# Performance work log

Hardware: AMD Instinct MI355X
Metric: run time of the kernel (lower is better)

Reference implementation:

```python
import jax, jax.numpy as jnp
import numpy as np

BERT_VOCAB_SIZE = 28996
INPUT_SIZE = 768
HIDDEN = 512
BI_H = 2 * HIDDEN


def _gru_cell(x, h, wih, whh, bih, bhh):
    # PyTorch GRUCell math. x: [I], h: [H]; wih: [3H, I], whh: [3H, H]
    H = h.shape[-1]
    gx = wih @ x + bih            # [3H]
    gh = whh @ h + bhh            # [3H]
    r = jax.nn.sigmoid(gx[:H] + gh[:H])
    z = jax.nn.sigmoid(gx[H:2 * H] + gh[H:2 * H])
    n = jnp.tanh(gx[2 * H:] + r * gh[2 * H:])
    return (1.0 - z) * n + z * h


def _run_gru(xs, h0, wih, whh, bih, bhh):
    def step(h, x):
        hn = _gru_cell(x, h, wih, whh, bih, bhh)
        return hn, hn
    _, hs = jax.lax.scan(step, h0, xs)
    return hs  # [L, H]


def setup_inputs() -> dict:
    key = jax.random.key(0)
    ks = jax.random.split(key, 16)
    s = 0.02
    inp = {
        'input_context': jax.random.normal(ks[0], (512, INPUT_SIZE), jnp.float32),
        'output_context': jax.random.normal(ks[1], (1024, INPUT_SIZE), jnp.float32),
        # forward encoder GRUCell
        'fw_wih': jax.random.normal(ks[2], (3 * HIDDEN, INPUT_SIZE), jnp.float32) * s,
        'fw_whh': jax.random.normal(ks[3], (3 * HIDDEN, HIDDEN), jnp.float32) * s,
        'fw_bih': jnp.zeros((3 * HIDDEN,), jnp.float32),
        'fw_bhh': jnp.zeros((3 * HIDDEN,), jnp.float32),
        # backward encoder GRUCell
        'bw_wih': jax.random.normal(ks[4], (3 * HIDDEN, INPUT_SIZE), jnp.float32) * s,
        'bw_whh': jax.random.normal(ks[5], (3 * HIDDEN, HIDDEN), jnp.float32) * s,
        'bw_bih': jnp.zeros((3 * HIDDEN,), jnp.float32),
        'bw_bhh': jnp.zeros((3 * HIDDEN,), jnp.float32),
        # decoder GRUCell (hidden = 2H)
        'dec_wih': jax.random.normal(ks[6], (3 * BI_H, INPUT_SIZE), jnp.float32) * s,
        'dec_whh': jax.random.normal(ks[7], (3 * BI_H, BI_H), jnp.float32) * s,
        'dec_bih': jnp.zeros((3 * BI_H,), jnp.float32),
        'dec_bhh': jnp.zeros((3 * BI_H,), jnp.float32),
        # vocab projection
        'W_pred': jax.random.normal(ks[8], (BI_H, BERT_VOCAB_SIZE), jnp.float32) * s,
    }
    return inp


def reference(input_context, output_context,
              fw_wih, fw_whh, fw_bih, fw_bhh,
              bw_wih, bw_whh, bw_bih, bw_bhh,
              dec_wih, dec_whh, dec_bih, dec_bhh,
              W_pred):
    h0 = jnp.zeros((HIDDEN,), input_context.dtype)
    # bidirectional encoder
    fwd_hs = _run_gru(input_context, h0, fw_wih, fw_whh, fw_bih, fw_bhh)        # [L, H]
    bwd_hs = _run_gru(input_context[::-1], h0, bw_wih, bw_whh, bw_bih, bw_bhh)[::-1]
    # column L-1 of cat((fwd, bwd), dim=0) -> [fwd_hs[-1]; bwd_hs[-1]]
    h_dec0 = jnp.concatenate([fwd_hs[-1], bwd_hs[-1]], axis=0)                   # [2H]
    # decoder inputs: step 0 uses output_context[0], step i>0 uses output_context[i-1]
    dec_in = jnp.concatenate([output_context[:1], output_context[:-1]], axis=0)  # [Lo, I]
    dec_hs = _run_gru(dec_in, h_dec0, dec_wih, dec_whh, dec_bih, dec_bhh)        # [Lo, 2H]
    preds = dec_hs @ W_pred                                                      # [Lo, V]
    return preds
```

## Files before the change

### kernel.cpp

```cpp
#include <hip/hip_runtime.h>
#include <math.h>


typedef unsigned long long u64;
typedef unsigned short ushort_t;
typedef __attribute__((ext_vector_type(8))) short short8;
typedef __attribute__((ext_vector_type(4))) float f32x4;

#define NV 28996
#define NRWG 64
#define NWORK 192
#define GXT 192
#define TRT 7264
#define VOCT 1816

__device__ __forceinline__ float sigmoidf_(float x) {
  return 1.0f / (1.0f + __expf(-x));
}
__device__ __forceinline__ float tanhf_(float x) {
  const float xx = fminf(fmaxf(x, -15.0f), 15.0f);
  const float e = __expf(2.0f * xx);
  return (e - 1.0f) / (e + 1.0f);
}
__device__ __forceinline__ ushort_t f2bf(float f) {
  union { float f; unsigned u; } c; c.f = f;
  unsigned u = c.u;
  u += 0x7fffu + ((u >> 16) & 1u);
  return (ushort_t)(u >> 16);
}

__device__ __forceinline__ u64 pack_ht(float h, unsigned tag) {
  union { float f; unsigned u; } c; c.f = h;
  return ((u64)tag << 32) | (u64)c.u;
}
__device__ __forceinline__ float pk_h(u64 v) {
  union { unsigned u; float f; } c; c.u = (unsigned)v; return c.f;
}
__device__ __forceinline__ void astore(u64* p, u64 v) {
  __hip_atomic_store(p, v, __ATOMIC_RELAXED, __HIP_MEMORY_SCOPE_AGENT);
}
__device__ __forceinline__ u64 aload(const u64* p) {
  return __hip_atomic_load((u64*)p, __ATOMIC_RELAXED, __HIP_MEMORY_SCOPE_AGENT);
}
__device__ __forceinline__ void astore32(unsigned* p, unsigned v) {
  __hip_atomic_store(p, v, __ATOMIC_RELAXED, __HIP_MEMORY_SCOPE_AGENT);
}
__device__ __forceinline__ unsigned aload32(const unsigned* p) {
  return __hip_atomic_load((unsigned*)p, __ATOMIC_RELAXED, __HIP_MEMORY_SCOPE_AGENT);
}
__device__ __forceinline__ void afadd32(unsigned* p, unsigned v) {
  __hip_atomic_fetch_add(p, v, __ATOMIC_RELAXED, __HIP_MEMORY_SCOPE_AGENT);
}
__device__ __forceinline__ u64 packf2(float a, float b) {
  union { float f; unsigned u; } ca, cb; ca.f = a; cb.f = b;
  return ((u64)cb.u << 32) | (u64)ca.u;
}

__global__ __launch_bounds__(512) void recur_fused(
    const float* __restrict__ gxfw,
    const float* __restrict__ gxdec,
    const float* __restrict__ gxbw,
    const float* __restrict__ whh_fw,
    const float* __restrict__ bhh_fw,
    const float* __restrict__ whh_dec,
    const float* __restrict__ bhh_dec,
    const float* __restrict__ bhh_bw,
    u64* fwbuf,
    u64* decbuf,
    unsigned* progress,
    unsigned* gx_done,
    unsigned* tr_done,
    float* dec_hs,
    unsigned* dec_hs_b32,
    const float* __restrict__ output_context,
    const float* __restrict__ dec_wih,
    const float* __restrict__ dec_bih,
    const float* __restrict__ W_pred,
    ushort_t* Wt,
    float* __restrict__ outC,
    float* gxdec_w,
    int do_bf16, int gx_expected)
{
  __shared__ __align__(16) char SMEM[36864];
  const int tid = threadIdx.x;
  const int wg = blockIdx.x;
  const int wave = tid >> 6;
  const int lane = tid & 63;

  if (wg < NRWG) {
    float* Hs = (float*)SMEM;

    if (wg == 0) {
      const int j = tid;
      const float r = sigmoidf_(gxbw[j] + bhh_bw[j]);
      const float z = sigmoidf_(gxbw[512 + j] + bhh_bw[512 + j]);
      const float n = tanhf_(gxbw[1024 + j] + r * bhh_bw[1024 + j]);
      astore(&decbuf[512 + j], pack_ht((1.0f - z) * n, 512u));
    }

    {
      const int u = (wg << 3) + wave;
      const float br = bhh_fw[u], bz = bhh_fw[512 + u], bn = bhh_fw[1024 + u];
      float4 wr[3][2];
#pragma unroll
      for (int g = 0; g < 3; ++g) {
        const float* w = whh_fw + (size_t)(g * 512 + u) * 512;
#pragma unroll
        for (int i = 0; i < 2; ++i)
          wr[g][i] = *(const float4*)&w[(i << 8) + (lane << 2)];
      }
      for (int t = 0; t < 512; ++t) {
        const u64* src = fwbuf + ((t & 1) << 9);
        float* hs = Hs + ((t & 1) << 9);
        if (wave == 0) {
          u64 v[8];
          for (;;) {
            bool ok = true;
#pragma unroll
            for (int j = 0; j < 8; ++j) {
              v[j] = aload(src + (j << 6) + lane);
              ok &= ((unsigned)(v[j] >> 32) >= (unsigned)t);
            }
            if (__all(ok)) break;
          }
#pragma unroll
          for (int j = 0; j < 8; ++j) hs[(j << 6) + lane] = pk_h(v[j]);
        }
        const float* gx = gxfw + (size_t)t * 1536;
        const float g0 = gx[u], g1 = gx[512 + u], g2 = gx[1024 + u];
        __syncthreads();
        const float4 ha = *(const float4*)&hs[lane << 2];
        const float4 hb = *(const float4*)&hs[256 + (lane << 2)];
        float p0 = wr[0][0].x * ha.x + wr[0][0].y * ha.y + wr[0][0].z * ha.z +
                   wr[0][0].w * ha.w + wr[0][1].x * hb.x + wr[0][1].y * hb.y +
                   wr[0][1].z * hb.z + wr[0][1].w * hb.w;
        float p1 = wr[1][0].x * ha.x + wr[1][0].y * ha.y + wr[1][0].z * ha.z +
                   wr[1][0].w * ha.w + wr[1][1].x * hb.x + wr[1][1].y * hb.y +
                   wr[1][1].z * hb.z + wr[1][1].w * hb.w;
        float p2 = wr[2][0].x * ha.x + wr[2][0].y * ha.y + wr[2][0].z * ha.z +
                   wr[2][0].w * ha.w + wr[2][1].x * hb.x + wr[2][1].y * hb.y +
                   wr[2][1].z * hb.z + wr[2][1].w * hb.w;
#pragma unroll
        for (int s = 1; s < 64; s <<= 1) {
          p0 += __shfl_xor(p0, s, 64);
          p1 += __shfl_xor(p1, s, 64);
          p2 += __shfl_xor(p2, s, 64);
        }
        if (lane == 0) {
          const float hold = hs[u];
          const float r = sigmoidf_(g0 + p0 + br);
          const float z = sigmoidf_(g1 + p1 + bz);
          const float n = tanhf_(g2 + r * (p2 + bn));
          const float hnew = (1.0f - z) * n + z * hold;
          if (t < 511)
            astore(fwbuf + (((t + 1) & 1) << 9) + u,
                   pack_ht(hnew, (unsigned)(t + 1)));
          else
            astore(decbuf + u, pack_ht(hnew, 512u));
        }
      }
    }
    __syncthreads();
    if (tid == 0 && gx_expected) {
      while (aload32(gx_done) < (unsigned)gx_expected)
        __builtin_amdgcn_s_sleep(8);
    }
    __syncthreads();

    {
      const int u0 = (wg << 4) + (wave << 1);
      float bb0[2], bb1[2], bb2[2];
      float4 wr[2][3][4];
#pragma unroll
      for (int uu = 0; uu < 2; ++uu) {
        bb0[uu] = bhh_dec[u0 + uu];
        bb1[uu] = bhh_dec[1024 + u0 + uu];
        bb2[uu] = bhh_dec[2048 + u0 + uu];
#pragma unroll
        for (int g = 0; g < 3; ++g) {
          const float* w = whh_dec + (size_t)(g * 1024 + u0 + uu) * 1024;
#pragma unroll
          for (int i = 0; i < 4; ++i)
            wr[uu][g][i] = *(const float4*)&w[(i << 8) + (lane << 2)];
        }
      }
      for (int td = 0; td < 1024; ++td) {
        const int t = 512 + td;
        const u64* src = decbuf + ((t & 1) << 10);
        float* hs = (float*)SMEM + ((t & 1) << 10);
        if (wave == 0) {
          u64 v[16];
          for (;;) {
            bool ok = true;
#pragma unroll
            for (int j = 0; j < 16; ++j) {
              v[j] = aload(src + (j << 6) + lane);
              ok &= ((unsigned)(v[j] >> 32) >= (unsigned)t);
            }
            if (__all(ok)) break;
          }
#pragma unroll
          for (int j = 0; j < 16; ++j) hs[(j << 6) + lane] = pk_h(v[j]);
        }
        const float* gx = gxdec + (size_t)td * 3072;
        float ga[2], gb[2], gc[2];
#pragma unroll
        for (int uu = 0; uu < 2; ++uu) {
          ga[uu] = gx[u0 + uu];
          gb[uu] = gx[1024 + u0 + uu];
          gc[uu] = gx[2048 + u0 + uu];
        }
        __syncthreads();
        if (wave == 7 && lane == 0 && td)
          astore32(progress + wg, (unsigned)td);
        float4 h4[4];
#pragma unroll
        for (int i = 0; i < 4; ++i)
          h4[i] = *(const float4*)&hs[(i << 8) + (lane << 2)];
        float hn0v = 0.f, hn1v = 0.f;
#pragma unroll
        for (int uu = 0; uu < 2; ++uu) {
          float p0 = 0.f, p1 = 0.f, p2 = 0.f;
#pragma unroll
          for (int i = 0; i < 4; ++i) {
            p0 += wr[uu][0][i].x * h4[i].x + wr[uu][0][i].y * h4[i].y +
                  wr[uu][0][i].z * h4[i].z + wr[uu][0][i].w * h4[i].w;
            p1 += wr[uu][1][i].x * h4[i].x + wr[uu][1][i].y * h4[i].y +
                  wr[uu][1][i].z * h4[i].z + wr[uu][1][i].w * h4[i].w;
            p2 += wr[uu][2][i].x * h4[i].x + wr[uu][2][i].y * h4[i].y +
                  wr[uu][2][i].z * h4[i].z + wr[uu][2][i].w * h4[i].w;
          }
#pragma unroll
          for (int s = 1; s < 64; s <<= 1) {
            p0 += __shfl_xor(p0, s, 64);
            p1 += __shfl_xor(p1, s, 64);
            p2 += __shfl_xor(p2, s, 64);
          }
          if (lane == 0) {
            const int u = u0 + uu;
            const float hold = hs[u];
            const float r = sigmoidf_(ga[uu] + p0 + bb0[uu]);
            const float z = sigmoidf_(gb[uu] + p1 + bb1[uu]);
            const float n = tanhf_(gc[uu] + r * (p2 + bb2[uu]));
            const float hnew = (1.0f - z) * n + z * hold;
            astore(decbuf + (((t + 1) & 1) << 10) + u,
                   pack_ht(hnew, (unsigned)(t + 1)));
            if (uu == 0) hn0v = hnew; else hn1v = hnew;
          }
        }
        if (lane == 0) {
          if (do_bf16) {
            const unsigned pk =
                (unsigned)f2bf(hn0v) | ((unsigned)f2bf(hn1v) << 16);
            astore32(&dec_hs_b32[(size_t)td * 512 + (u0 >> 1)], pk);
          } else {
            dec_hs[(size_t)td * 1024 + u0] = hn0v;
            dec_hs[(size_t)td * 1024 + u0 + 1] = hn1v;
          }
        }
      }
      __syncthreads();
      if (wave == 7 && lane == 0) astore32(progress + wg, 1024u);
    }
    return;
  }

  if (!do_bf16) return;
  const int wid = wg - NRWG;

  {
    float (*As)[132] = (float(*)[132])SMEM;
    float (*Bs)[132] = (float(*)[132])(SMEM + 16 * 132 * 4);
    const int cb = wid % 24, rb = wid / 24;
    const int n0 = cb * 128, m0 = rb * 128;
    float acc[8][8];
    if (tid < 256) {
#pragma unroll
      for (int i = 0; i < 8; ++i)
#pragma unroll
        for (int j = 0; j < 8; ++j) acc[i][j] = 0.f;
    }
    const int fl = tid >> 1, fk = (tid & 1) << 3;
    const int am = m0 + fl;
    const int asrow = (am == 0) ? 0 : am - 1;
    for (int k0 = 0; k0 < 768; k0 += 16) {
      if (tid < 256) {
        {
          const float* p = output_context + (size_t)asrow * 768 + k0 + fk;
          const float4 v0 = *(const float4*)p;
          const float4 v1 = *(const float4*)(p + 4);
          As[fk + 0][fl] = v0.x; As[fk + 1][fl] = v0.y;
          As[fk + 2][fl] = v0.z; As[fk + 3][fl] = v0.w;
          As[fk + 4][fl] = v1.x; As[fk + 5][fl] = v1.y;
          As[fk + 6][fl] = v1.z; As[fk + 7][fl] = v1.w;
        }
        {
          const float* p = dec_wih + (size_t)(n0 + fl) * 768 + k0 + fk;
          const float4 v0 = *(const float4*)p;
          const float4 v1 = *(const float4*)(p + 4);
          Bs[fk + 0][fl] = v0.x; Bs[fk + 1][fl] = v0.y;
          Bs[fk + 2][fl] = v0.z; Bs[fk + 3][fl] = v0.w;
          Bs[fk + 4][fl] = v1.x; Bs[fk + 5][fl] = v1.y;
          Bs[fk + 6][fl] = v1.z; Bs[fk + 7][fl] = v1.w;
        }
      }
      __syncthreads();
      if (tid < 256) {
        const int tx = tid & 15, ty = tid >> 4;
#pragma unroll
        for (int k = 0; k < 16; ++k) {
          const float4 a0 = *(const float4*)&As[k][ty << 3];
          const float4 a1 = *(const float4*)&As[k][(ty << 3) + 4];
          const float4 b0 = *(const float4*)&Bs[k][tx << 3];
          const float4 b1 = *(const float4*)&Bs[k][(tx << 3) + 4];
          const float av[8] = {a0.x, a0.y, a0.z, a0.w, a1.x, a1.y, a1.z, a1.w};
          const float bv[8] = {b0.x, b0.y, b0.z, b0.w, b1.x, b1.y, b1.z, b1.w};
#pragma unroll
          for (int i = 0; i < 8; ++i)
#pragma unroll
            for (int j = 0; j < 8; ++j) acc[i][j] += av[i] * bv[j];
        }
      }
      __syncthreads();
    }
    if (tid < 256) {
      const int tx = tid & 15, ty = tid >> 4;
      const int mb = m0 + (ty << 3), nb = n0 + (tx << 3);
#pragma unroll
      for (int i = 0; i < 8; ++i) {
        const int m = mb + i;
#pragma unroll
        for (int j = 0; j < 8; j += 2) {
          const float oa = acc[i][j] + dec_bih[nb + j];
          const float ob = acc[i][j + 1] + dec_bih[nb + j + 1];
          astore((u64*)&gxdec_w[(size_t)m * 3072 + nb + j], packf2(oa, ob));
        }
      }
    }
    __syncthreads();
    if (tid == 0) afadd32(gx_done, 1u);
  }

  {
    float (*T)[65] = (float(*)[65])SMEM;
    for (int i = wid; i < TRT; i += NWORK) {
      const int n0 = (i % 454) * 64;
      const int k0 = (i / 454) * 64;
      __syncthreads();
      if (tid < 256) {
        const int nloc = tid & 63, q = tid >> 6;
        const bool nok = (n0 + nloc) < NV;
#pragma unroll
        for (int r = 0; r < 16; ++r) {
          const int kloc = q + r * 4;
          T[kloc][nloc] =
              nok ? W_pred[(size_t)(k0 + kloc) * NV + n0 + nloc] : 0.f;
        }
      }
      __syncthreads();
      if (tid < 256) {
        const int nloc = tid >> 2;
        const int jb = (tid & 3) << 3;
        if (n0 + nloc < NV) {
          unsigned* dst =
              (unsigned*)Wt + (size_t)(n0 + nloc) * 512 + (k0 >> 1) + jb;
#pragma unroll
          for (int j = 0; j < 8; ++j) {
            const int kk = (jb + j) << 1;
            const unsigned pk = (unsigned)f2bf(T[kk][nloc]) |
                                ((unsigned)f2bf(T[kk + 1][nloc]) << 16);
            astore32(dst + j, pk);
          }
        }
      }
    }
    __syncthreads();
    if (tid == 0) afadd32(tr_done, 1u);
  }

  {
    if (wave == 0) {
      if (lane == 0)
        while (aload32(tr_done) < (unsigned)NWORK) __builtin_amdgcn_s_sleep(64);
    }
    __syncthreads();
    short* As = (short*)SMEM;
    short* Bs = As + 128 * 72;
    const ushort_t* A = (const ushort_t*)dec_hs_b32;
    const int wm = (tid >> 6) >> 1, wn = (tid >> 6) & 1;
    for (int i = wid; i < VOCT; i += NWORK) {
      const int rb = i / 227, cb = i % 227;
      const unsigned tgt = (unsigned)(rb * 128 + 128);
      if (wave == 0) {
        for (;;) {
          const unsigned p = aload32(progress + lane);
          if (__all(p >= tgt)) break;
          __builtin_amdgcn_s_sleep(64);
        }
      }
      __syncthreads();
      const int n0 = cb * 128, m0 = rb * 128;
      const int frow = tid >> 2;
      const int fko = (tid & 3) << 4;
      const bool bok = (n0 + frow) < NV;
      f32x4 acc[2][4];
#pragma unroll
      for (int a = 0; a < 2; ++a)
#pragma unroll
        for (int b = 0; b < 4; ++b) acc[a][b] = (f32x4){0.f, 0.f, 0.f, 0.f};
      for (int k0 = 0; k0 < 1024; k0 += 64) {
        {
          const uint4* s =
              (const uint4*)(A + (size_t)(m0 + frow) * 1024 + k0 + fko);
          uint4* d = (uint4*)&As[frow * 72 + fko];
          d[0] = s[0]; d[1] = s[1];
        }
        {
          uint4 v0 = make_uint4(0, 0, 0, 0), v1 = v0;
          if (bok) {
            const uint4* s =
                (const uint4*)(Wt + (size_t)(n0 + frow) * 1024 + k0 + fko);
            v0 = s[0]; v1 = s[1];
          }
          uint4* d = (uint4*)&Bs[frow * 72 + fko];
          d[0] = v0; d[1] = v1;
        }
        __syncthreads();
#pragma unroll
        for (int ks = 0; ks < 64; ks += 32) {
          short8 a[2], b[4];
#pragma unroll
          for (int fm = 0; fm < 2; ++fm)
            a[fm] = *(const short8*)&As[(wm * 32 + fm * 16 + (lane & 15)) * 72 +
                                        ks + ((lane >> 4) << 3)];
#pragma unroll
          for (int fn = 0; fn < 4; ++fn)
            b[fn] = *(const short8*)&Bs[(wn * 64 + fn * 16 + (lane & 15)) * 72 +
                                        ks + ((lane >> 4) << 3)];
#pragma unroll
          for (int fm = 0; fm < 2; ++fm)
#pragma unroll
            for (int fn = 0; fn < 4; ++fn)
              acc[fm][fn] = __builtin_amdgcn_mfma_f32_16x16x32_bf16(
                  a[fm], b[fn], acc[fm][fn], 0, 0, 0);
        }
        __syncthreads();
      }
#pragma unroll
      for (int fm = 0; fm < 2; ++fm) {
#pragma unroll
        for (int fn = 0; fn < 4; ++fn) {
          const int col = n0 + wn * 64 + fn * 16 + (lane & 15);
          if (col < NV) {
            const int rbase = m0 + wm * 32 + fm * 16 + ((lane >> 4) << 2);
#pragma unroll
            for (int r = 0; r < 4; ++r)
              outC[(size_t)(rbase + r) * NV + col] = acc[fm][fn][r];
          }
        }
      }
    }
  }
}

#define GBK 16
#define GLDS 132

template <int BT>
__global__ __launch_bounds__(256) void gemm128(
    const float* __restrict__ A, const float* __restrict__ B,
    const float* __restrict__ bias, float* __restrict__ C, int M, int N, int K,
    int rowmode, int fixedrow) {
  __shared__ float As[GBK][GLDS];
  __shared__ float Bs[GBK][GLDS];
  const int tid = threadIdx.x;
  const int n0 = blockIdx.x * 128;
  const int m0 = blockIdx.y * 128;
  const int tx = tid & 15;
  const int ty = tid >> 4;
  float acc[8][8];
#pragma unroll
  for (int i = 0; i < 8; ++i)
#pragma unroll
    for (int j = 0; j < 8; ++j) acc[i][j] = 0.f;

  const int fl = tid >> 1;
  const int fk = (tid & 1) << 3;
  const int am = m0 + fl;
  int asrow = am;
  if (rowmode == 1) asrow = (am == 0) ? 0 : am - 1;
  else if (rowmode == 2) asrow = fixedrow;
  const bool aok = (am < M);
  const bool nfull = (n0 + 128 <= N);

  for (int k0 = 0; k0 < K; k0 += GBK) {
    {
      float4 v0 = make_float4(0.f, 0.f, 0.f, 0.f), v1 = v0;
      if (aok) {
        const float* p = A + (size_t)asrow * K + k0 + fk;
        v0 = *(const float4*)p;
        v1 = *(const float4*)(p + 4);
      }
      As[fk + 0][fl] = v0.x; As[fk + 1][fl] = v0.y;
      As[fk + 2][fl] = v0.z; As[fk + 3][fl] = v0.w;
      As[fk + 4][fl] = v1.x; As[fk + 5][fl] = v1.y;
      As[fk + 6][fl] = v1.z; As[fk + 7][fl] = v1.w;
    }
    if (BT) {
      const int bn = n0 + fl;
      float4 v0 = make_float4(0.f, 0.f, 0.f, 0.f), v1 = v0;
      if (bn < N) {
        const float* p = B + (size_t)bn * K + k0 + fk;
        v0 = *(const float4*)p;
        v1 = *(const float4*)(p + 4);
      }
      Bs[fk + 0][fl] = v0.x; Bs[fk + 1][fl] = v0.y;
      Bs[fk + 2][fl] = v0.z; Bs[fk + 3][fl] = v0.w;
      Bs[fk + 4][fl] = v1.x; Bs[fk + 5][fl] = v1.y;
      Bs[fk + 6][fl] = v1.z; Bs[fk + 7][fl] = v1.w;
    } else {
      const int kl = tid >> 4;
      const int nq = (tid & 15) << 3;
      const float* p = B + (size_t)(k0 + kl) * N + n0 + nq;
      if (nfull) {
        *(float4*)&Bs[kl][nq] = *(const float4*)p;
        *(float4*)&Bs[kl][nq + 4] = *(const float4*)(p + 4);
      } else {
#pragma unroll
        for (int j = 0; j < 8; ++j)
          Bs[kl][nq + j] = (n0 + nq + j < N) ? p[j] : 0.f;
      }
    }
    __syncthreads();
#pragma unroll
    for (int k = 0; k < GBK; ++k) {
      const float4 a0 = *(const float4*)&As[k][ty << 3];
      const float4 a1 = *(const float4*)&As[k][(ty << 3) + 4];
      const float4 b0 = *(const float4*)&Bs[k][tx << 3];
      const float4 b1 = *(const float4*)&Bs[k][(tx << 3) + 4];
      const float av[8] = {a0.x, a0.y, a0.z, a0.w, a1.x, a1.y, a1.z, a1.w};
      const float bv[8] = {b0.x, b0.y, b0.z, b0.w, b1.x, b1.y, b1.z, b1.w};
#pragma unroll
      for (int i = 0; i < 8; ++i)
#pragma unroll
        for (int j = 0; j < 8; ++j) acc[i][j] += av[i] * bv[j];
    }
    __syncthreads();
  }

  const int mb = m0 + (ty << 3);
  const int nb = n0 + (tx << 3);
#pragma unroll
  for (int i = 0; i < 8; ++i) {
    const int m = mb + i;
    if (m >= M) continue;
    float o[8];
#pragma unroll
    for (int j = 0; j < 8; ++j) o[j] = acc[i][j];
    if (nfull) {
      if (bias) {
#pragma unroll
        for (int j = 0; j < 8; ++j) o[j] += bias[nb + j];
      }
      *(float4*)&C[(size_t)m * N + nb] = make_float4(o[0], o[1], o[2], o[3]);
      *(float4*)&C[(size_t)m * N + nb + 4] = make_float4(o[4], o[5], o[6], o[7]);
    } else {
#pragma unroll
      for (int j = 0; j < 8; ++j) {
        const int n = nb + j;
        if (n < N) C[(size_t)m * N + n] = o[j] + (bias ? bias[n] : 0.f);
      }
    }
  }
}

extern "C" void kernel_launch(void* const* d_in, const int* in_sizes, int n_in,
                              void* d_out, int out_size, void* d_ws,
                              size_t ws_size, hipStream_t stream) {
  (void)in_sizes; (void)n_in; (void)out_size;
  const float* input_context  = (const float*)d_in[0];
  const float* output_context = (const float*)d_in[1];
  const float* fw_wih = (const float*)d_in[2];
  const float* fw_whh = (const float*)d_in[3];
  const float* fw_bih = (const float*)d_in[4];
  const float* fw_bhh = (const float*)d_in[5];
  const float* bw_wih = (const float*)d_in[6];
  const float* bw_bih = (const float*)d_in[8];
  const float* bw_bhh = (const float*)d_in[9];
  const float* dec_wih = (const float*)d_in[10];
  const float* dec_whh = (const float*)d_in[11];
  const float* dec_bih = (const float*)d_in[12];
  const float* dec_bhh = (const float*)d_in[13];
  const float* W_pred  = (const float*)d_in[14];
  float* out = (float*)d_out;

  char* wsb = (char*)d_ws;
  u64* fwbuf   = (u64*)wsb;
  u64* decbuf  = (u64*)(wsb + 8192);
  unsigned* progress = (unsigned*)(wsb + 24576);
  unsigned* gx_done  = (unsigned*)(wsb + 24576 + 256);
  unsigned* tr_done  = (unsigned*)(wsb + 24576 + 260);
  float* gxbw  = (float*)(wsb + 25088);
  float* gxfw  = (float*)(wsb + 31232);
  float* gxdec = (float*)(wsb + 3176960);
  float* dec_hs = (float*)(wsb + 15759872);
  unsigned* dec_hs_b32 = (unsigned*)(wsb + 15759872);
  ushort_t* Wt = (ushort_t*)(wsb + 19954176);
  const int do_bf16 = (ws_size >= 79337984u) ? 1 : 0;

  hipMemsetAsync(d_ws, 0, 25088, stream);

  const dim3 blk(256);
  gemm128<1><<<dim3(12, 4), blk, 0, stream>>>(
      input_context, fw_wih, fw_bih, gxfw, 512, 1536, 768, 0, 0);
  gemm128<1><<<dim3(12, 1), blk, 0, stream>>>(
      input_context, bw_wih, bw_bih, gxbw, 1, 1536, 768, 2, 511);
  if (!do_bf16)
    gemm128<1><<<dim3(24, 8), blk, 0, stream>>>(
        output_context, dec_wih, dec_bih, gxdec, 1024, 3072, 768, 1, 0);

  const int grid = do_bf16 ? (NRWG + NWORK) : NRWG;
  recur_fused<<<dim3(grid), dim3(512), 0, stream>>>(
      gxfw, gxdec, gxbw, fw_whh, fw_bhh, dec_whh, dec_bhh, bw_bhh,
      fwbuf, decbuf, progress, gx_done, tr_done, dec_hs, dec_hs_b32,
      output_context, dec_wih, dec_bih, W_pred, Wt, out, gxdec,
      do_bf16, do_bf16 ? NWORK : 0);

  if (!do_bf16)
    gemm128<0><<<dim3(227, 8), blk, 0, stream>>>(
        dec_hs, W_pred, nullptr, out, 1024, NV, 1024, 0, 0);
}
```

Measured before the change: 5.201 ms.

## Fuse forward and backward input projections into the persistent recurrence kernel

Measured after the change: 4.980 ms. 1.04x faster.

```diff
diff --git a/kernel.cpp b/kernel.cpp
--- a/kernel.cpp
+++ b/kernel.cpp
@@ -10,7 +10,6 @@
 #define NV 28996
 #define NRWG 64
 #define NWORK 192
-#define GXT 192
 #define TRT 7264
 #define VOCT 1816
 
@@ -57,14 +56,17 @@
 }
 
 __global__ __launch_bounds__(512) void recur_fused(
-    const float* __restrict__ gxfw,
+    const float* __restrict__ input_context,
+    const float* __restrict__ fw_wih,
+    const float* __restrict__ fw_bih,
+    const float* __restrict__ bw_wih,
+    const float* __restrict__ bw_bih,
+    const float* __restrict__ bhh_bw,
     const float* __restrict__ gxdec,
-    const float* __restrict__ gxbw,
     const float* __restrict__ whh_fw,
     const float* __restrict__ bhh_fw,
     const float* __restrict__ whh_dec,
     const float* __restrict__ bhh_dec,
-    const float* __restrict__ bhh_bw,
     u64* fwbuf,
     u64* decbuf,
     unsigned* progress,
@@ -81,7 +83,7 @@
     float* gxdec_w,
     int do_bf16, int gx_expected)
 {
-  __shared__ __align__(16) char SMEM[36864];
+  __shared__ __align__(16) char SMEM[57344];
   const int tid = threadIdx.x;
   const int wg = blockIdx.x;
   const int wave = tid >> 6;
@@ -89,17 +91,64 @@
 
   if (wg < NRWG) {
     float* Hs = (float*)SMEM;
-
-    if (wg == 0) {
-      const int j = tid;
-      const float r = sigmoidf_(gxbw[j] + bhh_bw[j]);
-      const float z = sigmoidf_(gxbw[512 + j] + bhh_bw[512 + j]);
-      const float n = tanhf_(gxbw[1024 + j] + r * bhh_bw[1024 + j]);
-      astore(&decbuf[512 + j], pack_ht((1.0f - z) * n, 512u));
-    }
+    float* gxs = (float*)(SMEM + 8192);
+    const int u0 = wg << 3;
 
     {
-      const int u = (wg << 3) + wave;
+      const int r = (wave << 6) + lane;
+      const float* inrow = input_context + (size_t)r * 768;
+      const float* wbase = fw_wih + (size_t)u0 * 768;
+      float acc[24];
+#pragma unroll
+      for (int c = 0; c < 24; ++c) acc[c] = 0.f;
+      for (int k = 0; k < 768; k += 4) {
+        const float4 in4 = *(const float4*)&inrow[k];
+#pragma unroll
+        for (int u8 = 0; u8 < 8; ++u8) {
+#pragma unroll
+          for (int g = 0; g < 3; ++g) {
+            const float4 w4 =
+                *(const float4*)&wbase[(size_t)(g * 512 + u8) * 768 + k];
+            acc[u8 * 3 + g] +=
+                w4.x * in4.x + w4.y * in4.y + w4.z * in4.z + w4.w * in4.w;
+          }
+        }
+      }
+#pragma unroll
+      for (int u8 = 0; u8 < 8; ++u8)
+#pragma unroll
+        for (int g = 0; g < 3; ++g)
+          gxs[r * 24 + u8 * 3 + g] =
+              acc[u8 * 3 + g] + fw_bih[g * 512 + u0 + u8];
+    }
+    {
+      const int u = u0 + wave;
+      const float* in511 = input_context + (size_t)511 * 768;
+      float b0 = 0.f, b1 = 0.f, b2 = 0.f;
+      for (int k = lane; k < 768; k += 64) {
+        const float x = in511[k];
+        b0 += x * bw_wih[(size_t)u * 768 + k];
+        b1 += x * bw_wih[(size_t)(512 + u) * 768 + k];
+        b2 += x * bw_wih[(size_t)(1024 + u) * 768 + k];
+      }
+#pragma unroll
+      for (int s = 1; s < 64; s <<= 1) {
+        b0 += __shfl_xor(b0, s, 64);
+        b1 += __shfl_xor(b1, s, 64);
+        b2 += __shfl_xor(b2, s, 64);
+      }
+      if (lane == 0) {
+        const float r = sigmoidf_(b0 + bw_bih[u] + bhh_bw[u]);
+        const float z = sigmoidf_(b1 + bw_bih[512 + u] + bhh_bw[512 + u]);
+        const float n =
+            tanhf_(b2 + bw_bih[1024 + u] + r * bhh_bw[1024 + u]);
+        astore(&decbuf[512 + u], pack_ht((1.0f - z) * n, 512u));
+      }
+    }
+    __syncthreads();
+
+    {
+      const int u = u0 + wave;
       const float br = bhh_fw[u], bz = bhh_fw[512 + u], bn = bhh_fw[1024 + u];
       float4 wr[3][2];
 #pragma unroll
@@ -126,8 +175,9 @@
 #pragma unroll
           for (int j = 0; j < 8; ++j) hs[(j << 6) + lane] = pk_h(v[j]);
         }
-        const float* gx = gxfw + (size_t)t * 1536;
-        const float g0 = gx[u], g1 = gx[512 + u], g2 = gx[1024 + u];
+        const float g0 = gxs[t * 24 + wave * 3 + 0];
+        const float g1 = gxs[t * 24 + wave * 3 + 1];
+        const float g2 = gxs[t * 24 + wave * 3 + 2];
         __syncthreads();
         const float4 ha = *(const float4*)&hs[lane << 2];
         const float4 hb = *(const float4*)&hs[256 + (lane << 2)];
@@ -168,17 +218,17 @@
     __syncthreads();
 
     {
-      const int u0 = (wg << 4) + (wave << 1);
+      const int du0 = (wg << 4) + (wave << 1);
       float bb0[2], bb1[2], bb2[2];
       float4 wr[2][3][4];
 #pragma unroll
       for (int uu = 0; uu < 2; ++uu) {
-        bb0[uu] = bhh_dec[u0 + uu];
-        bb1[uu] = bhh_dec[1024 + u0 + uu];
-        bb2[uu] = bhh_dec[2048 + u0 + uu];
+        bb0[uu] = bhh_dec[du0 + uu];
+        bb1[uu] = bhh_dec[1024 + du0 + uu];
+        bb2[uu] = bhh_dec[2048 + du0 + uu];
 #pragma unroll
         for (int g = 0; g < 3; ++g) {
-          const float* w = whh_dec + (size_t)(g * 1024 + u0 + uu) * 1024;
+          const float* w = whh_dec + (size_t)(g * 1024 + du0 + uu) * 1024;
 #pragma unroll
           for (int i = 0; i < 4; ++i)
             wr[uu][g][i] = *(const float4*)&w[(i << 8) + (lane << 2)];
@@ -206,9 +256,9 @@
         float ga[2], gb[2], gc[2];
 #pragma unroll
         for (int uu = 0; uu < 2; ++uu) {
-          ga[uu] = gx[u0 + uu];
-          gb[uu] = gx[1024 + u0 + uu];
-          gc[uu] = gx[2048 + u0 + uu];
+          ga[uu] = gx[du0 + uu];
+          gb[uu] = gx[1024 + du0 + uu];
+          gc[uu] = gx[2048 + du0 + uu];
         }
         __syncthreads();
         if (wave == 7 && lane == 0 && td)
@@ -237,7 +287,7 @@
             p2 += __shfl_xor(p2, s, 64);
           }
           if (lane == 0) {
-            const int u = u0 + uu;
+            const int u = du0 + uu;
             const float hold = hs[u];
             const float r = sigmoidf_(ga[uu] + p0 + bb0[uu]);
             const float z = sigmoidf_(gb[uu] + p1 + bb1[uu]);
@@ -252,10 +302,10 @@
           if (do_bf16) {
             const unsigned pk =
                 (unsigned)f2bf(hn0v) | ((unsigned)f2bf(hn1v) << 16);
-            astore32(&dec_hs_b32[(size_t)td * 512 + (u0 >> 1)], pk);
+            astore32(&dec_hs_b32[(size_t)td * 512 + (du0 >> 1)], pk);
           } else {
-            dec_hs[(size_t)td * 1024 + u0] = hn0v;
-            dec_hs[(size_t)td * 1024 + u0 + 1] = hn1v;
+            dec_hs[(size_t)td * 1024 + du0] = hn0v;
+            dec_hs[(size_t)td * 1024 + du0 + 1] = hn1v;
           }
         }
       }
@@ -600,8 +650,6 @@
   unsigned* progress = (unsigned*)(wsb + 24576);
   unsigned* gx_done  = (unsigned*)(wsb + 24576 + 256);
   unsigned* tr_done  = (unsigned*)(wsb + 24576 + 260);
-  float* gxbw  = (float*)(wsb + 25088);
-  float* gxfw  = (float*)(wsb + 31232);
   float* gxdec = (float*)(wsb + 3176960);
   float* dec_hs = (float*)(wsb + 15759872);
   unsigned* dec_hs_b32 = (unsigned*)(wsb + 15759872);
@@ -610,23 +658,19 @@
 
   hipMemsetAsync(d_ws, 0, 25088, stream);
 
-  const dim3 blk(256);
-  gemm128<1><<<dim3(12, 4), blk, 0, stream>>>(
-      input_context, fw_wih, fw_bih, gxfw, 512, 1536, 768, 0, 0);
-  gemm128<1><<<dim3(12, 1), blk, 0, stream>>>(
-      input_context, bw_wih, bw_bih, gxbw, 1, 1536, 768, 2, 511);
   if (!do_bf16)
-    gemm128<1><<<dim3(24, 8), blk, 0, stream>>>(
+    gemm128<1><<<dim3(24, 8), dim3(256), 0, stream>>>(
         output_context, dec_wih, dec_bih, gxdec, 1024, 3072, 768, 1, 0);
 
   const int grid = do_bf16 ? (NRWG + NWORK) : NRWG;
   recur_fused<<<dim3(grid), dim3(512), 0, stream>>>(
-      gxfw, gxdec, gxbw, fw_whh, fw_bhh, dec_whh, dec_bhh, bw_bhh,
+      input_context, fw_wih, fw_bih, bw_wih, bw_bih, bw_bhh,
+      gxdec, fw_whh, fw_bhh, dec_whh, dec_bhh,
       fwbuf, decbuf, progress, gx_done, tr_done, dec_hs, dec_hs_b32,
       output_context, dec_wih, dec_bih, W_pred, Wt, out, gxdec,
       do_bf16, do_bf16 ? NWORK : 0);
 
   if (!do_bf16)
-    gemm128<0><<<dim3(227, 8), blk, 0, stream>>>(
+    gemm128<0><<<dim3(227, 8), dim3(256), 0, stream>>>(
         dec_hs, W_pred, nullptr, out, 1024, NV, 1024, 0, 0);
 }
```
